# Kernel optimization log

Measured on AMD Instinct MI355X. Metric: run time of the kernel, lower is better.

Reference implementation:

```python
import jax, jax.numpy as jnp
import numpy as np

DIST_THRESH = 0.1
W_DIST = 0.05
W_CHAMFER = 0.05
W_SEP = 0.0005


def setup_inputs() -> dict:
    key = jax.random.key(0)
    k1, k2, k3, k4 = jax.random.split(key, 4)
    B, N, K = 4, 200000, 64
    return {
        "landmarks_C": jax.random.uniform(k1, (B, N, 3), jnp.float32),          # predicted point coords
        "landmarks_F": jax.random.normal(k2, (B, N, 4), jnp.float32) * 0.05,    # [dist, dx, dy, dz]
        "targets_C": jax.random.uniform(k3, (B, K, 3), jnp.float32),            # GT landmark coords
        "targets_F": jax.random.randint(k4, (B, K), 0, 8),                      # GT landmark class labels
        "classes": jnp.arange(6),                                               # classes to supervise
    }


def reference(landmarks_C, landmarks_F, targets_C, targets_F, classes):
    def per_batch(C_i, F_i, tC, tF):
        # class mask over GT landmarks (replaces boolean indexing in torch)
        mask_k = jnp.any(tF[None, :] == classes[:, None], axis=0)          # [K]
        n_valid = mask_k.sum()
        dists_i = F_i[:, 0]                                                # predicted distance, [N]
        coords_i = C_i + F_i[:, 1:]                                        # refined coords, [N,3]
        # pairwise dists GT landmarks -> raw point coords, invalid classes pushed to +inf
        pd = jnp.linalg.norm(C_i[None, :, :] - tC[:, None, :], axis=-1)    # [K,N]
        pd = jnp.where(mask_k[:, None], pd, jnp.inf)
        min_d = pd.min(axis=0)                                             # [N]
        pm = min_d < DIST_THRESH                                           # points near some GT landmark
        # smooth-L1 (beta=1, sum) on predicted distance; clip(inf)=2*thresh reproduces empty-target fallback
        tgt = jnp.clip(min_d, 0.0, 2.0 * DIST_THRESH)
        diff = dists_i - tgt
        ad = jnp.abs(diff)
        dist_loss = jnp.where(ad < 1.0, 0.5 * diff * diff, ad - 0.5).sum()
        # pairwise dists GT landmarks -> refined coords
        ld = jnp.linalg.norm(coords_i[None, :, :] - tC[:, None, :], axis=-1)  # [K,N]
        ld_m = jnp.where(mask_k[:, None], ld, jnp.inf)
        p2g = jnp.where(pm, ld_m.min(axis=0), 0.0)                         # pred->gt, masked points only
        g2p = jnp.where(mask_k, ld_m.min(axis=1), 0.0)                     # gt->pred, valid GT only
        chamfer = (p2g * p2g).sum() + (g2p * g2p).sum()
        # separation: ratio of dists to 2 nearest (valid) GT landmarks, per masked point
        _, idx = jax.lax.top_k(-pd.T, 2)                                   # [N,2] indices of 2 smallest
        d01 = jnp.take_along_axis(ld.T, idx, axis=1)                       # [N,2]
        sep = jnp.where(pm, d01[:, 0] / d01[:, 1], 0.0).sum()
        sep = jnp.where(n_valid >= 2, sep, 0.0)
        return W_DIST * dist_loss + W_CHAMFER * chamfer + W_SEP * sep

    losses = jax.vmap(per_batch)(landmarks_C, landmarks_F, targets_C, targets_F)
    return losses.mean()
```

## Files before the change

### kernel.cpp

```cpp
#include <hip/hip_runtime.h>


constexpr int KT = 64;
constexpr int P  = 4;
constexpr int NREP = 16;
constexpr float DIST_THRESH = 0.1f;
constexpr float W_DIST    = 0.05f;
constexpr float W_CHAMFER = 0.05f;
constexpr float W_SEP     = 0.0005f;
constexpr float PT_SENT = -1e18f;
constexpr float TG_SENT = -1e18f;
constexpr float BIGF  = 3.0e38f;
constexpr float WBIAS = 16.0f;

__device__ __forceinline__ unsigned umin_(unsigned a, unsigned b) { return a < b ? a : b; }
__device__ __forceinline__ unsigned umax_(unsigned a, unsigned b) { return a > b ? a : b; }

__global__ __launch_bounds__(128, 6)
void landmark_main(const float* __restrict__ C, const float* __restrict__ F,
                   const float* __restrict__ tC, const int* __restrict__ tF,
                   const int* __restrict__ classes, int n_classes,
                   int N, unsigned int* __restrict__ g2p_rep,
                   float* __restrict__ sums_rep)
{
    __shared__ float4 tgtH2[2][64];
    __shared__ float4 tgtFull[KT];
    __shared__ uint4  mK1[64];
    __shared__ uint4  mK2[64];
    __shared__ float4 mLM[64];

    const int tid   = threadIdx.x;
    const int lane  = tid & 63;
    const int h     = tid >> 6;
    const int l31   = lane & 31;
    const int blk   = blockIdx.x;
    const int b     = blk & 3;
    const int chunk = blk >> 2;
    const int rep   = chunk & (NREP - 1);
    const int kbase = h << 5;

    if (tid < KT) {
        int f = tF[b * KT + tid];
        bool valid = false;
        for (int c = 0; c < n_classes; ++c) valid = valid || (f == classes[c]);
        float x = TG_SENT, y = TG_SENT, z = TG_SENT;
        if (valid) {
            x = tC[(b * KT + tid) * 3 + 0];
            y = tC[(b * KT + tid) * 3 + 1];
            z = tC[(b * KT + tid) * 3 + 2];
        }
        float4 v = make_float4(-2.f * x, -2.f * y, -2.f * z,
                               x * x + y * y + z * z + WBIAS);
        tgtFull[tid] = v;
        int hh = tid >> 5, j = tid & 31;
        tgtH2[hh][j] = v;
        tgtH2[hh][j + 32] = v;
    }
    __syncthreads();

    const float*  Cb = C + (size_t)b * N * 3;
    const float4* Fb = (const float4*)(F + (size_t)b * N * 4);
    const int base = chunk * (64 * P);

    float px[P], py[P], pz[P], ppm[P], cx[P], cy[P], cz[P], ccm[P], f0[P];
    bool  vp[P];
    #pragma unroll
    for (int p = 0; p < P; ++p) {
        int n = base + p * 64 + lane;
        bool v = (n < N);
        vp[p] = v;
        int ni = v ? n : 0;
        float4 f4 = Fb[ni];
        float X = Cb[3 * ni + 0], Y = Cb[3 * ni + 1], Z = Cb[3 * ni + 2];
        f0[p] = f4.x;
        if (!v) { X = PT_SENT; Y = PT_SENT; Z = PT_SENT; f4.y = f4.z = f4.w = 0.f; }
        px[p] = X;          py[p] = Y;          pz[p] = Z;
        cx[p] = X + f4.y;   cy[p] = Y + f4.z;   cz[p] = Z + f4.w;
        ppm[p] = fmaf(pz[p], pz[p], fmaf(py[p], py[p], px[p] * px[p])) - WBIAS;
        ccm[p] = fmaf(cz[p], cz[p], fmaf(cy[p], cy[p], cx[p] * cx[p])) - WBIAS;
    }

    unsigned k1[P], k2[P];
    float lmin[P];
    #pragma unroll
    for (int p = 0; p < P; ++p) { k1[p] = 0xFFFFFFFFu; k2[p] = 0xFFFFFFFFu; lmin[p] = BIGF; }

    float gmin = BIGF;
    const float4* TH = tgtH2[h];

    #pragma unroll 8
    for (int i = 0; i < 32; ++i) {
        const float4 T = TH[l31 + i];
        const unsigned kk = (unsigned)(kbase + ((l31 + i) & 31));
        float a[P];
        #pragma unroll
        for (int p = 0; p < P; ++p) {
            float keyf = fmaf(px[p], T.x, fmaf(py[p], T.y, fmaf(pz[p], T.z, T.w)));
            float ld2  = fmaf(cx[p], T.x, fmaf(cy[p], T.y, fmaf(cz[p], T.z, T.w)));
            unsigned key = (__float_as_uint(keyf) & 0xFFFFFFC0u) | kk;
            unsigned hi = umax_(k1[p], key);
            k1[p] = umin_(k1[p], key);
            k2[p] = umin_(k2[p], hi);
            lmin[p] = fminf(lmin[p], ld2);
            a[p] = ld2 + ccm[p];
        }
        float dl = fminf(fminf(a[0], a[1]), fminf(a[2], a[3]));
        int src = (l31 - i) & 31;
        float g1 = __shfl(dl, src, 64);
        float g2 = __shfl(dl, src + 32, 64);
        gmin = fminf(gmin, fminf(g1, g2));
    }

    if (h == 0) {
        mK1[lane] = make_uint4(k1[0], k1[1], k1[2], k1[3]);
        mK2[lane] = make_uint4(k2[0], k2[1], k2[2], k2[3]);
        mLM[lane] = make_float4(lmin[0], lmin[1], lmin[2], lmin[3]);
    }
    __syncthreads();

    if (lane < 32) {
        float g = fmaxf(gmin, 0.f);
        atomicMax(&g2p_rep[rep * 256 + b * 64 + kbase + lane], ~__float_as_uint(g));
    }

    if (h == 1) {
        uint4 A1 = mK1[lane], A2 = mK2[lane];
        float4 AL = mLM[lane];
        const unsigned a1v[P] = {A1.x, A1.y, A1.z, A1.w};
        const unsigned a2v[P] = {A2.x, A2.y, A2.z, A2.w};
        const float    alv[P] = {AL.x, AL.y, AL.z, AL.w};

        float dist_acc = 0.f, p2g_acc = 0.f, sep_acc = 0.f;
        #pragma unroll
        for (int p = 0; p < P; ++p) {
            unsigned m1 = umin_(a1v[p], k1[p]);
            unsigned m2 = umin_(umax_(a1v[p], k1[p]), umin_(a2v[p], k2[p]));
            float lm = fminf(alv[p], lmin[p]);
            float keyf1 = __uint_as_float(m1 & 0xFFFFFFC0u);
            float mind = sqrtf(fmaxf(keyf1 + ppm[p], 0.f));
            bool pm = (mind < DIST_THRESH) && vp[p];
            float tgtv = fminf(mind, 2.0f * DIST_THRESH);
            float diff = f0[p] - tgtv;
            float ad = fabsf(diff);
            float sl1 = (ad < 1.0f) ? 0.5f * diff * diff : (ad - 0.5f);
            if (vp[p]) dist_acc += sl1;
            if (pm) {
                p2g_acc += fmaxf(lm + ccm[p], 0.f);
                int i1 = (int)(m1 & 63u), i2 = (int)(m2 & 63u);
                float4 T1 = tgtFull[i1], T2 = tgtFull[i2];
                float l1sq = fmaf(cx[p], T1.x, fmaf(cy[p], T1.y, fmaf(cz[p], T1.z, T1.w))) + ccm[p];
                float l2sq = fmaf(cx[p], T2.x, fmaf(cy[p], T2.y, fmaf(cz[p], T2.z, T2.w))) + ccm[p];
                sep_acc += sqrtf(fmaxf(l1sq, 0.f) / fmaxf(l2sq, 1e-30f));
            }
        }

        float v0 = dist_acc, v1 = p2g_acc, v2 = sep_acc;
        #pragma unroll
        for (int o = 32; o > 0; o >>= 1) {
            v0 += __shfl_down(v0, o, 64);
            v1 += __shfl_down(v1, o, 64);
            v2 += __shfl_down(v2, o, 64);
        }
        if (lane == 0) {
            float* sb = sums_rep + rep * 16 + b;
            atomicAdd(sb + 0, v0);
            atomicAdd(sb + 4, v1);
            atomicAdd(sb + 8, v2);
        }
    }
}

__global__ void landmark_finalize(const int* __restrict__ tF, const int* __restrict__ classes,
                                  int n_classes, const unsigned int* __restrict__ g2p_rep,
                                  const float* __restrict__ sums_rep, float* __restrict__ out)
{
    __shared__ float lossb[4];
    const int tid = threadIdx.x;
    const int b = tid >> 6, k = tid & 63;

    int f = tF[b * KT + k];
    bool valid = false;
    for (int c = 0; c < n_classes; ++c) valid = valid || (f == classes[c]);

    unsigned enc = 0;
    for (int r = 0; r < NREP; ++r) enc = umax_(enc, g2p_rep[r * 256 + b * 64 + k]);
    float g  = valid ? __uint_as_float(~enc) : 0.f;
    float nv = valid ? 1.f : 0.f;

    #pragma unroll
    for (int o = 32; o > 0; o >>= 1) {
        g  += __shfl_down(g, o, 64);
        nv += __shfl_down(nv, o, 64);
    }
    if (k == 0) {
        float sd = 0.f, sp = 0.f, ss = 0.f;
        for (int r = 0; r < NREP; ++r) {
            sd += sums_rep[r * 16 + 0 + b];
            sp += sums_rep[r * 16 + 4 + b];
            ss += sums_rep[r * 16 + 8 + b];
        }
        float sep = (nv >= 2.f) ? ss : 0.f;
        lossb[b] = W_DIST * sd + W_CHAMFER * (sp + g) + W_SEP * sep;
    }
    __syncthreads();
    if (tid == 0)
        out[0] = (lossb[0] + lossb[1] + lossb[2] + lossb[3]) * 0.25f;
}

extern "C" void kernel_launch(void* const* d_in, const int* in_sizes, int n_in,
                              void* d_out, int out_size, void* d_ws, size_t ws_size,
                              hipStream_t stream)
{
    const float* C       = (const float*)d_in[0];
    const float* F       = (const float*)d_in[1];
    const float* tC      = (const float*)d_in[2];
    const int*   tF      = (const int*)d_in[3];
    const int*   classes = (const int*)d_in[4];
    const int n_classes = in_sizes[4];
    const int B = 4;
    const int N = in_sizes[0] / (3 * B);

    unsigned int* g2p_rep  = (unsigned int*)d_ws;
    float*        sums_rep = (float*)((char*)d_ws + NREP * 256 * 4);

    hipMemsetAsync(d_ws, 0, NREP * 256 * 4 + NREP * 16 * 4, stream);

    const int cpb = (N + 64 * P - 1) / (64 * P);
    landmark_main<<<cpb * 4, 128, 0, stream>>>(C, F, tC, tF, classes, n_classes,
                                               N, g2p_rep, sums_rep);
    landmark_finalize<<<1, 256, 0, stream>>>(tF, classes, n_classes, g2p_rep,
                                             sums_rep, (float*)d_out);
}
```

Baseline: 108.2 us.

## Pack raw and refined coords into packed FMA and reduce g2p via LDS atomics

```diff
diff --git a/kernel.cpp b/kernel.cpp
--- a/kernel.cpp
+++ b/kernel.cpp
@@ -13,8 +13,18 @@
 constexpr float BIGF  = 3.0e38f;
 constexpr float WBIAS = 16.0f;
 
+typedef float f2 __attribute__((ext_vector_type(2)));
+
 __device__ __forceinline__ unsigned umin_(unsigned a, unsigned b) { return a < b ? a : b; }
 __device__ __forceinline__ unsigned umax_(unsigned a, unsigned b) { return a > b ? a : b; }
+
+__device__ __forceinline__ f2 pk_fma(f2 a, f2 b, f2 c) {
+#if __has_builtin(__builtin_elementwise_fma)
+    return __builtin_elementwise_fma(a, b, c);
+#else
+    f2 r; r.x = fmaf(a.x, b.x, c.x); r.y = fmaf(a.y, b.y, c.y); return r;
+#endif
+}
 
 __global__ __launch_bounds__(128, 6)
 void landmark_main(const float* __restrict__ C, const float* __restrict__ F,
@@ -23,8 +33,9 @@
                    int N, unsigned int* __restrict__ g2p_rep,
                    float* __restrict__ sums_rep)
 {
-    __shared__ float4 tgtH2[2][64];
+    __shared__ float4 tgtH[2][32];
     __shared__ float4 tgtFull[KT];
+    __shared__ unsigned g2pLDS[KT];
     __shared__ uint4  mK1[64];
     __shared__ uint4  mK2[64];
     __shared__ float4 mLM[64];
@@ -37,7 +48,7 @@
     const int b     = blk & 3;
     const int chunk = blk >> 2;
     const int rep   = chunk & (NREP - 1);
-    const int kbase = h << 5;
+    const unsigned kbase = (unsigned)(h << 5);
 
     if (tid < KT) {
         int f = tF[b * KT + tid];
@@ -52,9 +63,8 @@
         float4 v = make_float4(-2.f * x, -2.f * y, -2.f * z,
                                x * x + y * y + z * z + WBIAS);
         tgtFull[tid] = v;
-        int hh = tid >> 5, j = tid & 31;
-        tgtH2[hh][j] = v;
-        tgtH2[hh][j + 32] = v;
+        tgtH[tid >> 5][tid & 31] = v;
+        g2pLDS[tid] = 0x7F7FFFFFu;
     }
     __syncthreads();
 
@@ -62,7 +72,8 @@
     const float4* Fb = (const float4*)(F + (size_t)b * N * 4);
     const int base = chunk * (64 * P);
 
-    float px[P], py[P], pz[P], ppm[P], cx[P], cy[P], cz[P], ccm[P], f0[P];
+    f2 pcx[P], pcy[P], pcz[P];
+    float ppm[P], ccm[P], f0[P];
     bool  vp[P];
     #pragma unroll
     for (int p = 0; p < P; ++p) {
@@ -74,10 +85,12 @@
         float X = Cb[3 * ni + 0], Y = Cb[3 * ni + 1], Z = Cb[3 * ni + 2];
         f0[p] = f4.x;
         if (!v) { X = PT_SENT; Y = PT_SENT; Z = PT_SENT; f4.y = f4.z = f4.w = 0.f; }
-        px[p] = X;          py[p] = Y;          pz[p] = Z;
-        cx[p] = X + f4.y;   cy[p] = Y + f4.z;   cz[p] = Z + f4.w;
-        ppm[p] = fmaf(pz[p], pz[p], fmaf(py[p], py[p], px[p] * px[p])) - WBIAS;
-        ccm[p] = fmaf(cz[p], cz[p], fmaf(cy[p], cy[p], cx[p] * cx[p])) - WBIAS;
+        float cxv = X + f4.y, cyv = Y + f4.z, czv = Z + f4.w;
+        pcx[p] = (f2){X, cxv};
+        pcy[p] = (f2){Y, cyv};
+        pcz[p] = (f2){Z, czv};
+        ppm[p] = fmaf(Z, Z, fmaf(Y, Y, X * X)) - WBIAS;
+        ccm[p] = fmaf(czv, czv, fmaf(cyv, cyv, cxv * cxv)) - WBIAS;
     }
 
     unsigned k1[P], k2[P];
@@ -85,30 +98,27 @@
     #pragma unroll
     for (int p = 0; p < P; ++p) { k1[p] = 0xFFFFFFFFu; k2[p] = 0xFFFFFFFFu; lmin[p] = BIGF; }
 
-    float gmin = BIGF;
-    const float4* TH = tgtH2[h];
-
     #pragma unroll 8
     for (int i = 0; i < 32; ++i) {
-        const float4 T = TH[l31 + i];
-        const unsigned kk = (unsigned)(kbase + ((l31 + i) & 31));
-        float a[P];
+        const unsigned kk = (unsigned)(l31 ^ i);
+        const float4 T = tgtH[h][kk];
+        const unsigned tk = kk | kbase;
+        const f2 Tx = {T.x, T.x}, Ty = {T.y, T.y}, Tz = {T.z, T.z}, Tw = {T.w, T.w};
+        float a0, a1, a2, a3;
         #pragma unroll
         for (int p = 0; p < P; ++p) {
-            float keyf = fmaf(px[p], T.x, fmaf(py[p], T.y, fmaf(pz[p], T.z, T.w)));
-            float ld2  = fmaf(cx[p], T.x, fmaf(cy[p], T.y, fmaf(cz[p], T.z, T.w)));
-            unsigned key = (__float_as_uint(keyf) & 0xFFFFFFC0u) | kk;
+            f2 w = pk_fma(pcx[p], Tx, pk_fma(pcy[p], Ty, pk_fma(pcz[p], Tz, Tw)));
+            unsigned key = (__float_as_uint(w.x) & 0xFFFFFFC0u) | tk;
             unsigned hi = umax_(k1[p], key);
             k1[p] = umin_(k1[p], key);
             k2[p] = umin_(k2[p], hi);
-            lmin[p] = fminf(lmin[p], ld2);
-            a[p] = ld2 + ccm[p];
-        }
-        float dl = fminf(fminf(a[0], a[1]), fminf(a[2], a[3]));
-        int src = (l31 - i) & 31;
-        float g1 = __shfl(dl, src, 64);
-        float g2 = __shfl(dl, src + 32, 64);
-        gmin = fminf(gmin, fminf(g1, g2));
+            lmin[p] = fminf(lmin[p], w.y);
+            float av = w.y + ccm[p];
+            if (p == 0) a0 = av; else if (p == 1) a1 = av;
+            else if (p == 2) a2 = av; else a3 = av;
+        }
+        float dl = fmaxf(fminf(fminf(a0, a1), fminf(a2, a3)), 0.f);
+        atomicMin(&g2pLDS[tk], __float_as_uint(dl));
     }
 
     if (h == 0) {
@@ -118,12 +128,9 @@
     }
     __syncthreads();
 
-    if (lane < 32) {
-        float g = fmaxf(gmin, 0.f);
-        atomicMax(&g2p_rep[rep * 256 + b * 64 + kbase + lane], ~__float_as_uint(g));
-    }
-
-    if (h == 1) {
+    if (h == 0) {
+        atomicMax(&g2p_rep[rep * 256 + b * 64 + lane], ~g2pLDS[lane]);
+    } else {
         uint4 A1 = mK1[lane], A2 = mK2[lane];
         float4 AL = mLM[lane];
         const unsigned a1v[P] = {A1.x, A1.y, A1.z, A1.w};
@@ -148,8 +155,9 @@
                 p2g_acc += fmaxf(lm + ccm[p], 0.f);
                 int i1 = (int)(m1 & 63u), i2 = (int)(m2 & 63u);
                 float4 T1 = tgtFull[i1], T2 = tgtFull[i2];
-                float l1sq = fmaf(cx[p], T1.x, fmaf(cy[p], T1.y, fmaf(cz[p], T1.z, T1.w))) + ccm[p];
-                float l2sq = fmaf(cx[p], T2.x, fmaf(cy[p], T2.y, fmaf(cz[p], T2.z, T2.w))) + ccm[p];
+                float cxv = pcx[p].y, cyv = pcy[p].y, czv = pcz[p].y;
+                float l1sq = fmaf(cxv, T1.x, fmaf(cyv, T1.y, fmaf(czv, T1.z, T1.w))) + ccm[p];
+                float l2sq = fmaf(cxv, T2.x, fmaf(cyv, T2.y, fmaf(czv, T2.z, T2.w))) + ccm[p];
                 sep_acc += sqrtf(fmaxf(l1sq, 0.f) / fmaxf(l2sq, 1e-30f));
             }
         }
```

Result: faster. 99.29 us (-8.3%).
